# Performance work log

Measured on AMD Instinct MI355X. Metric: run time of the kernel, lower is better.

Reference implementation:

```python
import jax, jax.numpy as jnp
import numpy as np

NQ = 4
DIM = 2 ** NQ  # 16 basis states for the 4-qubit patch circuit


def _cnot_chain_perm():
    # Combined basis permutation for CNOT(0,1); CNOT(1,2); CNOT(2,3),
    # with wire i = bit (NQ-1-i) of the basis index (wire 0 most significant).
    idx = np.arange(DIM)
    perm = idx
    for c in range(NQ - 1):
        t = c + 1
        cbit = (idx >> (NQ - 1 - c)) & 1
        single = idx ^ (cbit << (NQ - 1 - t))  # involution: flip target iff control=1
        perm = perm[single]
    return perm

_BITS = np.array([[(b >> (NQ - 1 - i)) & 1 for i in range(NQ)] for b in range(DIM)])
CNOT_PERM = jnp.asarray(_cnot_chain_perm())
ZSIGN = jnp.asarray(1.0 - 2.0 * _BITS, dtype=jnp.float32)  # (DIM, NQ): PauliZ eigenvalues per basis/qubit


def _quantum(patches, params):
    """Exact statevector sim of: RY(x_i) -> CNOT chain -> RZ(p0) -> CNOT chain -> RZ(p1) -> <Z_i>.
    patches: (N, 4) angles; params: (2, 4). Returns (N, 4) expectation values."""
    half = 0.5 * patches
    amp = jnp.stack([jnp.cos(half), jnp.sin(half)], axis=-1)  # (N, 4, 2) per-qubit RY|0> amplitudes
    state = jnp.einsum('na,nb,nc,nd->nabcd', amp[:, 0], amp[:, 1], amp[:, 2], amp[:, 3])
    state = state.reshape(-1, DIM).astype(jnp.complex64)
    for row in range(2):
        state = state[:, CNOT_PERM]                    # CNOT chain = basis permutation
        phase = jnp.exp(-0.5j * (ZSIGN @ params[row]))  # RZ diagonal, shared across batch
        state = state * phase
    probs = jnp.real(state) ** 2 + jnp.imag(state) ** 2
    return probs @ ZSIGN  # (N, 4)


def setup_inputs() -> dict:
    key = jax.random.key(0)
    ks = jax.random.split(key, 5)
    B = 8192
    return {
        'x': jax.random.uniform(ks[0], (B, 1, 28, 28), jnp.float32),
        'params': jax.random.normal(ks[1], (2, NQ), jnp.float32),
        'W1': jax.random.normal(ks[2], (256, 784), jnp.float32) * 0.03,
        'b1': jnp.zeros((256,), jnp.float32),
        'W2': jax.random.normal(ks[3], (128, 256), jnp.float32) * 0.06,
        'b2': jnp.zeros((128,), jnp.float32),
        'W3': jax.random.normal(ks[4], (10, 128), jnp.float32) * 0.08,
        'b3': jnp.zeros((10,), jnp.float32),
    }


def reference(x, params, W1, b1, W2, b2, W3, b3):
    B = x.shape[0]
    # Extract 2x2 patches (row-major within patch, row-major patch order) -> (B*196, 4)
    patches = x[:, 0].reshape(B, 14, 2, 14, 2).transpose(0, 1, 3, 2, 4).reshape(B * 196, 4)
    feats = _quantum(patches, params).reshape(B, 196 * 4)  # cat of per-patch 4-vectors
    h = jax.nn.relu(feats @ W1.T + b1)   # Dropout is identity in eval mode
    h = jax.nn.relu(h @ W2.T + b2)
    logits = h @ W3.T + b3
    return jax.nn.log_softmax(logits, axis=-1)
```

## Files before the change

### kernel.cpp

```cpp
#include <hip/hip_runtime.h>
#include <stdint.h>

typedef __attribute__((ext_vector_type(8))) short short8;
typedef __attribute__((ext_vector_type(4))) float f32x4;

#define DEVI __device__ __forceinline__

DEVI ushort f2bf(float f) {
  union { float f; uint32_t u; } v; v.f = f;
  uint32_t r = v.u + 0x7fffu + ((v.u >> 16) & 1u);
  return (ushort)(r >> 16);
}

DEVI ushort4 pack4(float a, float b, float c, float d) {
  ushort4 o; o.x = f2bf(a); o.y = f2bf(b); o.z = f2bf(c); o.w = f2bf(d);
  return o;
}

__global__ __launch_bounds__(256) void gemm1_fused(
    const float* __restrict__ x, const float* __restrict__ W1,
    const float* __restrict__ b1, ushort* __restrict__ h1) {
  constexpr int LDA = 72;
  constexpr int NK = 13;
  __shared__ ushort As[2][64 * LDA];
  __shared__ ushort Bs[2][64 * LDA];

  const int tid = threadIdx.x;
  const int lane = tid & 63;
  const int w = tid >> 6, wm = w >> 1, wn = w & 1;
  const int bm = blockIdx.x & 127, bn = blockIdx.x >> 7;
  const int m0 = bm * 64, n0 = bn * 64;

  const int srow = tid >> 4;
  const int pl = tid & 15;
  const int kc4 = pl * 4;

  float2 atop[4], abot[4];
  float4 bw[4];

  f32x4 acc[2][2];
#pragma unroll
  for (int m = 0; m < 2; ++m)
#pragma unroll
    for (int n = 0; n < 2; ++n) {
      f32x4 z = {0.f, 0.f, 0.f, 0.f};
      acc[m][n] = z;
    }

  auto loadT = [&](int kt) {
    const int q = kt * 16 + pl;
    if (q < 196) {
      const int i = q / 14, j = q - i * 14;
      const float* px = x + i * 56 + j * 2;
#pragma unroll
      for (int c = 0; c < 4; ++c) {
        const float* p = px + (size_t)(m0 + c * 16 + srow) * 784;
        atop[c] = *(const float2*)p;
        abot[c] = *(const float2*)(p + 28);
      }
    }
    const int k0 = kt * 64;
    if (k0 + kc4 < 784) {
#pragma unroll
      for (int c = 0; c < 4; ++c)
        bw[c] = *(const float4*)(W1 + (size_t)(n0 + c * 16 + srow) * 784 + k0 + kc4);
    } else {
#pragma unroll
      for (int c = 0; c < 4; ++c) bw[c] = make_float4(0.f, 0.f, 0.f, 0.f);
    }
  };

  auto writeT = [&](int buf, int kt) {
    const int q = kt * 16 + pl;
    ushort* as = As[buf];
    ushort* bs = Bs[buf];
    if (q < 196) {
#pragma unroll
      for (int c = 0; c < 4; ++c) {
        float c0 = __cosf(atop[c].x), c1 = __cosf(atop[c].y);
        float c2 = __cosf(abot[c].x), c3 = __cosf(abot[c].y);
        *(ushort4*)(as + (c * 16 + srow) * LDA + pl * 4) =
            pack4(c0, c1, c0 * c2, c1 * c3);
      }
    } else {
      ushort4 z; z.x = 0; z.y = 0; z.z = 0; z.w = 0;
#pragma unroll
      for (int c = 0; c < 4; ++c)
        *(ushort4*)(as + (c * 16 + srow) * LDA + pl * 4) = z;
    }
#pragma unroll
    for (int c = 0; c < 4; ++c)
      *(ushort4*)(bs + (c * 16 + srow) * LDA + kc4) =
          pack4(bw[c].x, bw[c].y, bw[c].z, bw[c].w);
  };

  auto mma = [&](int buf) {
    const ushort* as = As[buf];
    const ushort* bs = Bs[buf];
#pragma unroll
    for (int ks = 0; ks < 2; ++ks) {
      short8 af[2], bf[2];
#pragma unroll
      for (int m = 0; m < 2; ++m) {
        int r = wm * 32 + m * 16 + (lane & 15);
        af[m] = *(const short8*)(as + r * LDA + ks * 32 + (lane >> 4) * 8);
      }
#pragma unroll
      for (int n = 0; n < 2; ++n) {
        int cdx = wn * 32 + n * 16 + (lane & 15);
        bf[n] = *(const short8*)(bs + cdx * LDA + ks * 32 + (lane >> 4) * 8);
      }
#pragma unroll
      for (int m = 0; m < 2; ++m)
#pragma unroll
        for (int n = 0; n < 2; ++n)
          acc[m][n] = __builtin_amdgcn_mfma_f32_16x16x32_bf16(af[m], bf[n], acc[m][n], 0, 0, 0);
    }
  };

  loadT(0);
  writeT(0, 0);
  __syncthreads();
  int cur = 0;
  for (int kt = 0; kt < NK; ++kt) {
    if (kt + 1 < NK) loadT(kt + 1);
    mma(cur);
    if (kt + 1 < NK) writeT(cur ^ 1, kt + 1);
    __syncthreads();
    cur ^= 1;
  }

#pragma unroll
  for (int m = 0; m < 2; ++m)
#pragma unroll
    for (int n = 0; n < 2; ++n) {
      int colg = n0 + wn * 32 + n * 16 + (lane & 15);
      float bval = b1[colg];
#pragma unroll
      for (int r = 0; r < 4; ++r) {
        int rowg = m0 + wm * 32 + m * 16 + (lane >> 4) * 4 + r;
        h1[(size_t)rowg * 256 + colg] = f2bf(fmaxf(acc[m][n][r] + bval, 0.f));
      }
    }
}

__global__ __launch_bounds__(256) void gemm2_head(
    const ushort* __restrict__ h1, const float* __restrict__ W2,
    const float* __restrict__ b2, const float* __restrict__ W3,
    const float* __restrict__ b3, float* __restrict__ out) {
  constexpr int LDA = 72;
  constexpr int NK = 4;
  __shared__ ushort As[2][32 * LDA];
  __shared__ ushort Bs[2][128 * LDA];
  __shared__ float h2f[32][132];
  __shared__ float W3s[1280];

  const int tid = threadIdx.x;
  const int lane = tid & 63;
  const int w = tid >> 6, wm = w >> 1, wn = w & 1;
  const int m0 = blockIdx.x * 32;

  for (int i = tid; i < 1280; i += 256) W3s[i] = W3[i];

  const int ar = tid >> 3, asl = tid & 7;
  const int br = tid >> 4, kc4 = (tid & 15) * 4;

  uint4 av;
  float4 bw[8];

  auto loadT = [&](int kt) {
    const int k0 = kt * 64;
    av = *(const uint4*)(h1 + (size_t)(m0 + ar) * 256 + k0 + asl * 8);
#pragma unroll
    for (int c = 0; c < 8; ++c)
      bw[c] = *(const float4*)(W2 + (size_t)(c * 16 + br) * 256 + k0 + kc4);
  };
  auto writeT = [&](int buf) {
    *(uint4*)(As[buf] + ar * LDA + asl * 8) = av;
#pragma unroll
    for (int c = 0; c < 8; ++c)
      *(ushort4*)(Bs[buf] + (c * 16 + br) * LDA + kc4) =
          pack4(bw[c].x, bw[c].y, bw[c].z, bw[c].w);
  };

  f32x4 acc[4];
#pragma unroll
  for (int n = 0; n < 4; ++n) {
    f32x4 z = {0.f, 0.f, 0.f, 0.f};
    acc[n] = z;
  }

  auto mma = [&](int buf) {
    const ushort* as = As[buf];
    const ushort* bs = Bs[buf];
#pragma unroll
    for (int ks = 0; ks < 2; ++ks) {
      int r = wm * 16 + (lane & 15);
      short8 af = *(const short8*)(as + r * LDA + ks * 32 + (lane >> 4) * 8);
#pragma unroll
      for (int n = 0; n < 4; ++n) {
        int cdx = wn * 64 + n * 16 + (lane & 15);
        short8 bf = *(const short8*)(bs + cdx * LDA + ks * 32 + (lane >> 4) * 8);
        acc[n] = __builtin_amdgcn_mfma_f32_16x16x32_bf16(af, bf, acc[n], 0, 0, 0);
      }
    }
  };

  loadT(0);
  writeT(0);
  __syncthreads();
  int cur = 0;
  for (int kt = 0; kt < NK; ++kt) {
    if (kt + 1 < NK) loadT(kt + 1);
    mma(cur);
    if (kt + 1 < NK) writeT(cur ^ 1);
    __syncthreads();
    cur ^= 1;
  }

#pragma unroll
  for (int n = 0; n < 4; ++n) {
    int col = wn * 64 + n * 16 + (lane & 15);
    float bval = b2[col];
#pragma unroll
    for (int r = 0; r < 4; ++r)
      h2f[wm * 16 + (lane >> 4) * 4 + r][col] = fmaxf(acc[n][r] + bval, 0.f);
  }
  __syncthreads();

  {
    int r = tid >> 3, p = tid & 7;
    float a10[10];
#pragma unroll
    for (int n = 0; n < 10; ++n) a10[n] = 0.f;
#pragma unroll
    for (int e = 0; e < 16; ++e) {
      int k = e * 8 + p;
      float hv = h2f[r][k];
#pragma unroll
      for (int n = 0; n < 10; ++n) a10[n] = fmaf(hv, W3s[n * 128 + k], a10[n]);
    }
#pragma unroll
    for (int n = 0; n < 10; ++n) {
      a10[n] += __shfl_xor(a10[n], 1);
      a10[n] += __shfl_xor(a10[n], 2);
      a10[n] += __shfl_xor(a10[n], 4);
    }
    if (p == 0) {
#pragma unroll
      for (int n = 0; n < 10; ++n) a10[n] += b3[n];
      float mx = a10[0];
#pragma unroll
      for (int n = 1; n < 10; ++n) mx = fmaxf(mx, a10[n]);
      float s = 0.f;
#pragma unroll
      for (int n = 0; n < 10; ++n) s += __expf(a10[n] - mx);
      float lse = mx + __logf(s);
      float* po = out + (size_t)(m0 + r) * 10;
#pragma unroll
      for (int n = 0; n < 10; ++n) po[n] = a10[n] - lse;
    }
  }
}

extern "C" void kernel_launch(void* const* d_in, const int* in_sizes, int n_in,
                              void* d_out, int out_size, void* d_ws, size_t ws_size,
                              hipStream_t stream) {
  const float* x  = (const float*)d_in[0];
  const float* W1 = (const float*)d_in[2];
  const float* b1 = (const float*)d_in[3];
  const float* W2 = (const float*)d_in[4];
  const float* b2 = (const float*)d_in[5];
  const float* W3 = (const float*)d_in[6];
  const float* b3 = (const float*)d_in[7];
  float* out = (float*)d_out;

  ushort* h1 = (ushort*)d_ws;

  hipLaunchKernelGGL(gemm1_fused, dim3(512), dim3(256), 0, stream, x, W1, b1, h1);
  hipLaunchKernelGGL(gemm2_head, dim3(256), dim3(256), 0, stream, h1, W2, b2, W3, b3, out);
}
```

Baseline: 30.88 us.

## Fuse both GEMMs and head into one kernel keeping h1 in LDS

Merges the two kernels into one 512-thread kernel. Each block owns 32 rows and the full 256-wide hidden layer, so h1 stays in shared memory instead of round-tripping through global memory, and one launch is removed. The LDS double buffering is replaced by single-buffered tiles with register prefetch and two barriers per step. Only 256 blocks run, so occupancy is lower. Every block also re-reads and converts all of W1 and W2, which adds redundant weight traffic.

```diff
diff --git a/kernel.cpp b/kernel.cpp
--- a/kernel.cpp
+++ b/kernel.cpp
@@ -17,26 +17,66 @@
   return o;
 }
 
-__global__ __launch_bounds__(256) void gemm1_fused(
+#define LDB 72
+#define H1LD 280
+
+__global__ __launch_bounds__(512, 2) void mega_kernel(
     const float* __restrict__ x, const float* __restrict__ W1,
-    const float* __restrict__ b1, ushort* __restrict__ h1) {
-  constexpr int LDA = 72;
-  constexpr int NK = 13;
-  __shared__ ushort As[2][64 * LDA];
-  __shared__ ushort Bs[2][64 * LDA];
+    const float* __restrict__ b1, const float* __restrict__ W2,
+    const float* __restrict__ b2, const float* __restrict__ W3,
+    const float* __restrict__ b3, float* __restrict__ out) {
+  __shared__ __align__(16) ushort As[32 * LDB];
+  __shared__ __align__(16) ushort Bs[256 * LDB];
+  __shared__ __align__(16) ushort h1t[32 * H1LD];
+  __shared__ __align__(16) float W3s[1280];
 
   const int tid = threadIdx.x;
   const int lane = tid & 63;
-  const int w = tid >> 6, wm = w >> 1, wn = w & 1;
-  const int bm = blockIdx.x & 127, bn = blockIdx.x >> 7;
-  const int m0 = bm * 64, n0 = bn * 64;
-
-  const int srow = tid >> 4;
-  const int pl = tid & 15;
-  const int kc4 = pl * 4;
-
-  float2 atop[4], abot[4];
-  float4 bw[4];
+  const int w = tid >> 6;
+  const int m0g = blockIdx.x * 32;
+
+  const int arow = tid >> 4, pl = tid & 15;
+
+  float2 xt, xb;
+  bool aval;
+  float4 bw[8];
+
+  auto loadA1 = [&](int kt) {
+    const int q = kt * 16 + pl;
+    aval = (q < 196);
+    if (aval) {
+      const int i = q / 14, j = q - i * 14;
+      const float* p = x + (size_t)(m0g + arow) * 784 + i * 56 + j * 2;
+      xt = *(const float2*)p;
+      xb = *(const float2*)(p + 28);
+    }
+  };
+  auto loadB1 = [&](int kt) {
+    const int k0 = kt * 64;
+#pragma unroll
+    for (int c = 0; c < 8; ++c) {
+      const int flat = c * 512 + tid, r = flat >> 4, sl = flat & 15;
+      if (k0 + sl * 4 < 784)
+        bw[c] = *(const float4*)(W1 + (size_t)r * 784 + k0 + sl * 4);
+      else
+        bw[c] = make_float4(0.f, 0.f, 0.f, 0.f);
+    }
+  };
+  auto writeT1 = [&]() {
+    if (aval) {
+      float c0 = __cosf(xt.x), c1 = __cosf(xt.y);
+      float c2 = __cosf(xb.x), c3 = __cosf(xb.y);
+      *(ushort4*)(As + arow * LDB + pl * 4) = pack4(c0, c1, c0 * c2, c1 * c3);
+    } else {
+      ushort4 z; z.x = 0; z.y = 0; z.z = 0; z.w = 0;
+      *(ushort4*)(As + arow * LDB + pl * 4) = z;
+    }
+#pragma unroll
+    for (int c = 0; c < 8; ++c) {
+      const int flat = c * 512 + tid, r = flat >> 4, sl = flat & 15;
+      *(ushort4*)(Bs + r * LDB + sl * 4) = pack4(bw[c].x, bw[c].y, bw[c].z, bw[c].w);
+    }
+  };
 
   f32x4 acc[2][2];
 #pragma unroll
@@ -47,196 +87,109 @@
       acc[m][n] = z;
     }
 
-  auto loadT = [&](int kt) {
-    const int q = kt * 16 + pl;
-    if (q < 196) {
-      const int i = q / 14, j = q - i * 14;
-      const float* px = x + i * 56 + j * 2;
-#pragma unroll
-      for (int c = 0; c < 4; ++c) {
-        const float* p = px + (size_t)(m0 + c * 16 + srow) * 784;
-        atop[c] = *(const float2*)p;
-        abot[c] = *(const float2*)(p + 28);
-      }
-    }
-    const int k0 = kt * 64;
-    if (k0 + kc4 < 784) {
-#pragma unroll
-      for (int c = 0; c < 4; ++c)
-        bw[c] = *(const float4*)(W1 + (size_t)(n0 + c * 16 + srow) * 784 + k0 + kc4);
-    } else {
-#pragma unroll
-      for (int c = 0; c < 4; ++c) bw[c] = make_float4(0.f, 0.f, 0.f, 0.f);
-    }
-  };
-
-  auto writeT = [&](int buf, int kt) {
-    const int q = kt * 16 + pl;
-    ushort* as = As[buf];
-    ushort* bs = Bs[buf];
-    if (q < 196) {
-#pragma unroll
-      for (int c = 0; c < 4; ++c) {
-        float c0 = __cosf(atop[c].x), c1 = __cosf(atop[c].y);
-        float c2 = __cosf(abot[c].x), c3 = __cosf(abot[c].y);
-        *(ushort4*)(as + (c * 16 + srow) * LDA + pl * 4) =
-            pack4(c0, c1, c0 * c2, c1 * c3);
-      }
-    } else {
-      ushort4 z; z.x = 0; z.y = 0; z.z = 0; z.w = 0;
-#pragma unroll
-      for (int c = 0; c < 4; ++c)
-        *(ushort4*)(as + (c * 16 + srow) * LDA + pl * 4) = z;
-    }
-#pragma unroll
-    for (int c = 0; c < 4; ++c)
-      *(ushort4*)(bs + (c * 16 + srow) * LDA + kc4) =
-          pack4(bw[c].x, bw[c].y, bw[c].z, bw[c].w);
-  };
-
-  auto mma = [&](int buf) {
-    const ushort* as = As[buf];
-    const ushort* bs = Bs[buf];
+  loadA1(0);
+  loadB1(0);
+  for (int kt = 0; kt < 13; ++kt) {
+    writeT1();
+    __syncthreads();
+    if (kt < 12) { loadA1(kt + 1); loadB1(kt + 1); }
 #pragma unroll
     for (int ks = 0; ks < 2; ++ks) {
       short8 af[2], bf[2];
 #pragma unroll
-      for (int m = 0; m < 2; ++m) {
-        int r = wm * 32 + m * 16 + (lane & 15);
-        af[m] = *(const short8*)(as + r * LDA + ks * 32 + (lane >> 4) * 8);
-      }
-#pragma unroll
-      for (int n = 0; n < 2; ++n) {
-        int cdx = wn * 32 + n * 16 + (lane & 15);
-        bf[n] = *(const short8*)(bs + cdx * LDA + ks * 32 + (lane >> 4) * 8);
-      }
+      for (int m = 0; m < 2; ++m)
+        af[m] = *(const short8*)(As + (m * 16 + (lane & 15)) * LDB + ks * 32 + (lane >> 4) * 8);
+#pragma unroll
+      for (int n = 0; n < 2; ++n)
+        bf[n] = *(const short8*)(Bs + (w * 32 + n * 16 + (lane & 15)) * LDB + ks * 32 + (lane >> 4) * 8);
 #pragma unroll
       for (int m = 0; m < 2; ++m)
 #pragma unroll
         for (int n = 0; n < 2; ++n)
           acc[m][n] = __builtin_amdgcn_mfma_f32_16x16x32_bf16(af[m], bf[n], acc[m][n], 0, 0, 0);
     }
-  };
-
-  loadT(0);
-  writeT(0, 0);
+    __syncthreads();
+  }
+
+#pragma unroll
+  for (int n = 0; n < 2; ++n) {
+    const int col = w * 32 + n * 16 + (lane & 15);
+    const float bval = b1[col];
+#pragma unroll
+    for (int m = 0; m < 2; ++m)
+#pragma unroll
+      for (int r = 0; r < 4; ++r) {
+        const int row = m * 16 + (lane >> 4) * 4 + r;
+        h1t[row * H1LD + col] = f2bf(fmaxf(acc[m][n][r] + bval, 0.f));
+      }
+  }
+  for (int i = tid; i < 1280; i += 512) W3s[i] = W3[i];
   __syncthreads();
-  int cur = 0;
-  for (int kt = 0; kt < NK; ++kt) {
-    if (kt + 1 < NK) loadT(kt + 1);
-    mma(cur);
-    if (kt + 1 < NK) writeT(cur ^ 1, kt + 1);
-    __syncthreads();
-    cur ^= 1;
-  }
-
-#pragma unroll
-  for (int m = 0; m < 2; ++m)
-#pragma unroll
-    for (int n = 0; n < 2; ++n) {
-      int colg = n0 + wn * 32 + n * 16 + (lane & 15);
-      float bval = b1[colg];
+
+  float4 bw2[4];
+  auto loadB2 = [&](int kt) {
+    const int k0 = kt * 64;
+#pragma unroll
+    for (int c = 0; c < 4; ++c) {
+      const int flat = c * 512 + tid, r = flat >> 4, sl = flat & 15;
+      bw2[c] = *(const float4*)(W2 + (size_t)r * 256 + k0 + sl * 4);
+    }
+  };
+  auto writeT2 = [&]() {
+#pragma unroll
+    for (int c = 0; c < 4; ++c) {
+      const int flat = c * 512 + tid, r = flat >> 4, sl = flat & 15;
+      *(ushort4*)(Bs + r * LDB + sl * 4) = pack4(bw2[c].x, bw2[c].y, bw2[c].z, bw2[c].w);
+    }
+  };
+
+  f32x4 acc2[2];
+#pragma unroll
+  for (int m = 0; m < 2; ++m) {
+    f32x4 z = {0.f, 0.f, 0.f, 0.f};
+    acc2[m] = z;
+  }
+
+  loadB2(0);
+  for (int kt = 0; kt < 4; ++kt) {
+    writeT2();
+    __syncthreads();
+    if (kt < 3) loadB2(kt + 1);
+#pragma unroll
+    for (int ks = 0; ks < 2; ++ks) {
+      short8 bf = *(const short8*)(Bs + (w * 16 + (lane & 15)) * LDB + ks * 32 + (lane >> 4) * 8);
+#pragma unroll
+      for (int m = 0; m < 2; ++m) {
+        short8 af = *(const short8*)(h1t + (m * 16 + (lane & 15)) * H1LD + kt * 64 + ks * 32 + (lane >> 4) * 8);
+        acc2[m] = __builtin_amdgcn_mfma_f32_16x16x32_bf16(af, bf, acc2[m], 0, 0, 0);
+      }
+    }
+    __syncthreads();
+  }
+
+  float* h2f = (float*)h1t;
+  {
+    const int col = w * 16 + (lane & 15);
+    const float bval = b2[col];
+#pragma unroll
+    for (int m = 0; m < 2; ++m)
 #pragma unroll
       for (int r = 0; r < 4; ++r) {
-        int rowg = m0 + wm * 32 + m * 16 + (lane >> 4) * 4 + r;
-        h1[(size_t)rowg * 256 + colg] = f2bf(fmaxf(acc[m][n][r] + bval, 0.f));
+        const int row = m * 16 + (lane >> 4) * 4 + r;
+        h2f[row * 132 + col] = fmaxf(acc2[m][r] + bval, 0.f);
       }
-    }
-}
-
-__global__ __launch_bounds__(256) void gemm2_head(
-    const ushort* __restrict__ h1, const float* __restrict__ W2,
-    const float* __restrict__ b2, const float* __restrict__ W3,
-    const float* __restrict__ b3, float* __restrict__ out) {
-  constexpr int LDA = 72;
-  constexpr int NK = 4;
-  __shared__ ushort As[2][32 * LDA];
-  __shared__ ushort Bs[2][128 * LDA];
-  __shared__ float h2f[32][132];
-  __shared__ float W3s[1280];
-
-  const int tid = threadIdx.x;
-  const int lane = tid & 63;
-  const int w = tid >> 6, wm = w >> 1, wn = w & 1;
-  const int m0 = blockIdx.x * 32;
-
-  for (int i = tid; i < 1280; i += 256) W3s[i] = W3[i];
-
-  const int ar = tid >> 3, asl = tid & 7;
-  const int br = tid >> 4, kc4 = (tid & 15) * 4;
-
-  uint4 av;
-  float4 bw[8];
-
-  auto loadT = [&](int kt) {
-    const int k0 = kt * 64;
-    av = *(const uint4*)(h1 + (size_t)(m0 + ar) * 256 + k0 + asl * 8);
-#pragma unroll
-    for (int c = 0; c < 8; ++c)
-      bw[c] = *(const float4*)(W2 + (size_t)(c * 16 + br) * 256 + k0 + kc4);
-  };
-  auto writeT = [&](int buf) {
-    *(uint4*)(As[buf] + ar * LDA + asl * 8) = av;
-#pragma unroll
-    for (int c = 0; c < 8; ++c)
-      *(ushort4*)(Bs[buf] + (c * 16 + br) * LDA + kc4) =
-          pack4(bw[c].x, bw[c].y, bw[c].z, bw[c].w);
-  };
-
-  f32x4 acc[4];
-#pragma unroll
-  for (int n = 0; n < 4; ++n) {
-    f32x4 z = {0.f, 0.f, 0.f, 0.f};
-    acc[n] = z;
-  }
-
-  auto mma = [&](int buf) {
-    const ushort* as = As[buf];
-    const ushort* bs = Bs[buf];
-#pragma unroll
-    for (int ks = 0; ks < 2; ++ks) {
-      int r = wm * 16 + (lane & 15);
-      short8 af = *(const short8*)(as + r * LDA + ks * 32 + (lane >> 4) * 8);
-#pragma unroll
-      for (int n = 0; n < 4; ++n) {
-        int cdx = wn * 64 + n * 16 + (lane & 15);
-        short8 bf = *(const short8*)(bs + cdx * LDA + ks * 32 + (lane >> 4) * 8);
-        acc[n] = __builtin_amdgcn_mfma_f32_16x16x32_bf16(af, bf, acc[n], 0, 0, 0);
-      }
-    }
-  };
-
-  loadT(0);
-  writeT(0);
+  }
   __syncthreads();
-  int cur = 0;
-  for (int kt = 0; kt < NK; ++kt) {
-    if (kt + 1 < NK) loadT(kt + 1);
-    mma(cur);
-    if (kt + 1 < NK) writeT(cur ^ 1);
-    __syncthreads();
-    cur ^= 1;
-  }
-
-#pragma unroll
-  for (int n = 0; n < 4; ++n) {
-    int col = wn * 64 + n * 16 + (lane & 15);
-    float bval = b2[col];
-#pragma unroll
-    for (int r = 0; r < 4; ++r)
-      h2f[wm * 16 + (lane >> 4) * 4 + r][col] = fmaxf(acc[n][r] + bval, 0.f);
-  }
-  __syncthreads();
 
   {
-    int r = tid >> 3, p = tid & 7;
+    const int r = tid >> 4, p = tid & 15;
     float a10[10];
 #pragma unroll
     for (int n = 0; n < 10; ++n) a10[n] = 0.f;
 #pragma unroll
-    for (int e = 0; e < 16; ++e) {
-      int k = e * 8 + p;
-      float hv = h2f[r][k];
+    for (int e = 0; e < 8; ++e) {
+      const int k = e * 16 + p;
+      const float hv = h2f[r * 132 + k];
 #pragma unroll
       for (int n = 0; n < 10; ++n) a10[n] = fmaf(hv, W3s[n * 128 + k], a10[n]);
     }
@@ -245,6 +198,7 @@
       a10[n] += __shfl_xor(a10[n], 1);
       a10[n] += __shfl_xor(a10[n], 2);
       a10[n] += __shfl_xor(a10[n], 4);
+      a10[n] += __shfl_xor(a10[n], 8);
     }
     if (p == 0) {
 #pragma unroll
@@ -255,8 +209,8 @@
       float s = 0.f;
 #pragma unroll
       for (int n = 0; n < 10; ++n) s += __expf(a10[n] - mx);
-      float lse = mx + __logf(s);
-      float* po = out + (size_t)(m0 + r) * 10;
+      const float lse = mx + __logf(s);
+      float* po = out + (size_t)(m0g + r) * 10;
 #pragma unroll
       for (int n = 0; n < 10; ++n) po[n] = a10[n] - lse;
     }
@@ -275,8 +229,6 @@
   const float* b3 = (const float*)d_in[7];
   float* out = (float*)d_out;
 
-  ushort* h1 = (ushort*)d_ws;
-
-  hipLaunchKernelGGL(gemm1_fused, dim3(512), dim3(256), 0, stream, x, W1, b1, h1);
-  hipLaunchKernelGGL(gemm2_head, dim3(256), dim3(256), 0, stream, h1, W2, b2, W3, b3, out);
-}
+  hipLaunchKernelGGL(mega_kernel, dim3(256), dim3(512), 0, stream,
+                     x, W1, b1, W2, b2, W3, b3, out);
+}
```

New measurement: 33.04 us. +7.0%, slower.
